# Optimization experiments

Hardware: AMD Instinct MI355X
Metric: run time of the kernel (lower is better)

The kernel has to match this reference:

```python
import jax, jax.numpy as jnp
import numpy as np

B, HW, N, C, F, ITERS = 32, 4096, 16, 128, 512, 3
EPS_LN = 1e-5
EPS_ATTN = 1e-5


def _ln(x, g, b):
    m = x.mean(-1, keepdims=True)
    v = ((x - m) ** 2).mean(-1, keepdims=True)
    return (x - m) / jnp.sqrt(v + EPS_LN) * g + b


def _gru(x, h, wih, whh, bih, bhh):
    # torch.nn.GRUCell math
    gi = x @ wih.T + bih
    gh = h @ whh.T + bhh
    i_r, i_z, i_n = jnp.split(gi, 3, axis=-1)
    h_r, h_z, h_n = jnp.split(gh, 3, axis=-1)
    r = jax.nn.sigmoid(i_r + h_r)
    z = jax.nn.sigmoid(i_z + h_z)
    n = jnp.tanh(i_n + r * h_n)
    return (1.0 - z) * n + z * h


def setup_inputs() -> dict:
    key = jax.random.key(0)
    ks = jax.random.split(key, 16)
    s = 0.02
    d = {
        'inp': jax.random.normal(ks[0], (B, HW, C), jnp.float32),
        'query': jax.random.normal(ks[1], (B, N, C), jnp.float32),
        'ln_kv_g': jnp.ones((C,), jnp.float32),
        'ln_kv_b': jnp.zeros((C,), jnp.float32),
        'Wk': jax.random.normal(ks[2], (C, C), jnp.float32) * s,
        'Wv': jax.random.normal(ks[3], (C, C), jnp.float32) * s,
        'ln_q_g': jnp.ones((C,), jnp.float32),
        'ln_q_b': jnp.zeros((C,), jnp.float32),
        'Wq': jax.random.normal(ks[4], (C, C), jnp.float32) * s,
        'gru_wih': jax.random.normal(ks[5], (3 * C, C), jnp.float32) * s,
        'gru_whh': jax.random.normal(ks[6], (3 * C, C), jnp.float32) * s,
        'gru_bih': jnp.zeros((3 * C,), jnp.float32),
        'gru_bhh': jnp.zeros((3 * C,), jnp.float32),
        'ln2_g': jnp.ones((C,), jnp.float32),
        'ln2_b': jnp.zeros((C,), jnp.float32),
        'ffn_w1': jax.random.normal(ks[7], (F, C), jnp.float32) * s,
        'ffn_b1': jnp.zeros((F,), jnp.float32),
        'ffn_w2': jax.random.normal(ks[8], (C, F), jnp.float32) * s,
        'ffn_b2': jnp.zeros((C,), jnp.float32),
    }
    return d


def reference(inp, query, ln_kv_g, ln_kv_b, Wk, Wv, ln_q_g, ln_q_b, Wq,
              gru_wih, gru_whh, gru_bih, gru_bhh, ln2_g, ln2_b,
              ffn_w1, ffn_b1, ffn_w2, ffn_b2):
    b, n, c = query.shape
    kv = _ln(inp, ln_kv_g, ln_kv_b)
    k = kv @ Wk.T  # (b, hw, c)
    v = kv @ Wv.T  # (b, hw, c)
    scale = c ** -0.5
    q = query
    a0 = None
    for _ in range(ITERS):
        x = q
        qn = _ln(q, ln_q_g, ln_q_b) @ Wq.T
        logit = jnp.einsum('bqc,bkc->bqk', qn * scale, k)  # (b, n, hw)
        a0 = jax.nn.softmax(logit, axis=1)  # inverted: softmax over slots
        a = a0 / (a0.sum(2, keepdims=True) + EPS_ATTN)  # renorm over keys
        u = jnp.einsum('bqk,bkc->bqc', a, v)
        y = _gru(u.reshape(b * n, c), x.reshape(b * n, c),
                 gru_wih, gru_whh, gru_bih, gru_bhh).reshape(b, n, c)
        z = _ln(y, ln2_g, ln2_b)
        ffn = jax.nn.relu(z @ ffn_w1.T + ffn_b1) @ ffn_w2.T + ffn_b2
        q = y + ffn
    return (q, a0)
```

## Files before the change

### kernel.cpp

```cpp
#include <hip/hip_runtime.h>
#include <math.h>

#define B_ 32
#define HW_ 4096
#define N_ 16
#define C_ 128
#define F_ 512
#define ITERS_ 3
#define EPS_LN 1e-5f
#define EPS_ATTN 1e-5f

typedef __attribute__((ext_vector_type(8))) short short8;
typedef __attribute__((ext_vector_type(4))) float f32x4;

static __device__ __forceinline__ unsigned short f2b(float f) {
    union { float f; unsigned u; } v; v.f = f;
    unsigned r = v.u + 0x7fffu + ((v.u >> 16) & 1u);
    return (unsigned short)(r >> 16);
}
static __device__ __forceinline__ float blo(unsigned u) {
    union { unsigned u; float f; } v; v.u = u << 16; return v.f;
}
static __device__ __forceinline__ float bhi(unsigned u) {
    union { unsigned u; float f; } v; v.u = u & 0xffff0000u; return v.f;
}

__global__ __launch_bounds__(256) void k_prep(
    const float* __restrict__ Wk, const float* __restrict__ Wv,
    const float* __restrict__ wih, const float* __restrict__ whh,
    const float* __restrict__ w1, const float* __restrict__ w2,
    unsigned short* __restrict__ Wk_bf, unsigned short* __restrict__ Wv_bf,
    unsigned short* __restrict__ wihT, unsigned short* __restrict__ whhT,
    unsigned short* __restrict__ w1T, unsigned short* __restrict__ w2T,
    const float* __restrict__ query, const float* __restrict__ lnqg,
    const float* __restrict__ lnqb, const float* __restrict__ Wq,
    float* __restrict__ wqTf, unsigned short* __restrict__ qn_g)
{
    __shared__ __align__(16) float xq[16 * 128];
    int tid = threadIdx.x;
    int blk = blockIdx.x;
    if (blk < 32) {
        int t = blk * 256 + tid;
        const float* src; unsigned short* dst; int off;
        if (t < 4096) { src = Wk; dst = Wk_bf; off = t; }
        else          { src = Wv; dst = Wv_bf; off = t - 4096; }
        float4 a = ((const float4*)src)[off];
        uint2 p;
        p.x = (unsigned)f2b(a.x) | ((unsigned)f2b(a.y) << 16);
        p.y = (unsigned)f2b(a.z) | ((unsigned)f2b(a.w) << 16);
        *(uint2*)(dst + off * 4) = p;
        return;
    }
    if (blk < 256) {
        const float* src; unsigned short* dst; int o, g, id, Cin;
        if (blk < 80) {
            id = (blk - 32) * 256 + tid;
            g = id / 384; o = id - g * 384;
            src = wih; dst = wihT; Cin = 128;
        } else if (blk < 128) {
            id = (blk - 80) * 256 + tid;
            g = id / 384; o = id - g * 384;
            src = whh; dst = whhT; Cin = 128;
        } else if (blk < 192) {
            id = (blk - 128) * 256 + tid;
            g = id >> 9; o = id & 511;
            src = w1; dst = w1T; Cin = 128;
        } else {
            id = (blk - 192) * 256 + tid;
            g = id >> 7; o = id & 127;
            src = w2; dst = w2T; Cin = 512;
        }
        float4 a = *(const float4*)(src + o * Cin + g * 4);
        uint2 p;
        p.x = (unsigned)f2b(a.x) | ((unsigned)f2b(a.y) << 16);
        p.y = (unsigned)f2b(a.z) | ((unsigned)f2b(a.w) << 16);
        *(uint2*)(dst + id * 4) = p;
        return;
    }
    if (blk >= 288) {
        int t = (blk - 288) * 256 + tid;
        int c = t & 127, g = t >> 7;
        float4 a = *(const float4*)(Wq + c * 128 + g * 4);
        ((float4*)wqTf)[g * 128 + c] = a;
        return;
    }
    int b = blk - 256;
    int n = tid >> 4, part = tid & 15;
    int row = b * 16 + n;
    const float4* x4 = (const float4*)(query + row * 128 + part * 8);
    float4 x0 = x4[0], x1 = x4[1];
    float s = x0.x + x0.y + x0.z + x0.w + x1.x + x1.y + x1.z + x1.w;
    float ss = x0.x * x0.x + x0.y * x0.y + x0.z * x0.z + x0.w * x0.w +
               x1.x * x1.x + x1.y * x1.y + x1.z * x1.z + x1.w * x1.w;
    s += __shfl_xor(s, 1); s += __shfl_xor(s, 2); s += __shfl_xor(s, 4); s += __shfl_xor(s, 8);
    ss += __shfl_xor(ss, 1); ss += __shfl_xor(ss, 2); ss += __shfl_xor(ss, 4); ss += __shfl_xor(ss, 8);
    float mean = s * (1.f / 128.f);
    float var = ss * (1.f / 128.f) - mean * mean;
    float rstd = rsqrtf(var + EPS_LN);
    const float4* g4 = (const float4*)(lnqg + part * 8);
    const float4* b4 = (const float4*)(lnqb + part * 8);
    float4 g0 = g4[0], g1 = g4[1], bb0 = b4[0], bb1 = b4[1];
    float4 o0, o1;
    o0.x = (x0.x - mean) * rstd * g0.x + bb0.x;
    o0.y = (x0.y - mean) * rstd * g0.y + bb0.y;
    o0.z = (x0.z - mean) * rstd * g0.z + bb0.z;
    o0.w = (x0.w - mean) * rstd * g0.w + bb0.w;
    o1.x = (x1.x - mean) * rstd * g1.x + bb1.x;
    o1.y = (x1.y - mean) * rstd * g1.y + bb1.y;
    o1.z = (x1.z - mean) * rstd * g1.z + bb1.z;
    o1.w = (x1.w - mean) * rstd * g1.w + bb1.w;
    float4* xrow = (float4*)&xq[n * 128];
    xrow[part * 2] = o0;
    xrow[part * 2 + 1] = o1;
    __syncthreads();
    float o[8] = {0.f, 0.f, 0.f, 0.f, 0.f, 0.f, 0.f, 0.f};
    const float4* xv4 = (const float4*)&xq[n * 128];
#pragma unroll 4
    for (int j = 0; j < 32; j++) {
        float4 xv = xv4[j];
#pragma unroll
        for (int i = 0; i < 8; i++) {
            float4 w = ((const float4*)(Wq + (part * 8 + i) * 128))[j];
            o[i] += w.x * xv.x + w.y * xv.y + w.z * xv.z + w.w * xv.w;
        }
    }
    const float scale = 0.08838834764831845f;
#pragma unroll
    for (int i = 0; i < 8; i++)
        qn_g[row * 128 + part * 8 + i] = f2b(o[i] * scale);
}

__global__ __launch_bounds__(256) void k_kvproj(
    const float* __restrict__ inp, const float* __restrict__ lng,
    const float* __restrict__ lnb, const unsigned short* __restrict__ Wk_bf,
    const unsigned short* __restrict__ Wv_bf, unsigned short* __restrict__ Kbf,
    unsigned short* __restrict__ Vt)
{
    __shared__ __align__(16) unsigned short W_lds[128 * 128];
    __shared__ __align__(16) unsigned short T_lds[8960];
    const int tid = threadIdx.x;
    const int wave = tid >> 6, lane = tid & 63;
    const int l15 = lane & 15, q4 = lane >> 4;
    const int kof = q4 * 8;
    const int tile0 = blockIdx.x * 64;
    const int b = tile0 >> 12;
    const int hwbase = tile0 & (HW_ - 1);

    const int srow = tid >> 1, shalf = tid & 1;
    const int sswz = srow & 7;

    float x[4][8];
    {
        const float* rowp = inp + (tile0 + (wave << 4) + l15) * C_;
        float s = 0.f, ss = 0.f;
#pragma unroll
        for (int ks = 0; ks < 4; ks++) {
#pragma unroll
            for (int h = 0; h < 2; h++) {
                float4 v = *(const float4*)(rowp + ks * 32 + kof + h * 4);
                x[ks][h * 4 + 0] = v.x; x[ks][h * 4 + 1] = v.y;
                x[ks][h * 4 + 2] = v.z; x[ks][h * 4 + 3] = v.w;
                s += v.x + v.y + v.z + v.w;
                ss += v.x * v.x + v.y * v.y + v.z * v.z + v.w * v.w;
            }
        }
        s += __shfl_xor(s, 16);  s += __shfl_xor(s, 32);
        ss += __shfl_xor(ss, 16); ss += __shfl_xor(ss, 32);
        float mean = s * (1.f / 128.f);
        float var = ss * (1.f / 128.f) - mean * mean;
        float rstd = rsqrtf(var + EPS_LN);
#pragma unroll
        for (int ks = 0; ks < 4; ks++) {
#pragma unroll
            for (int h = 0; h < 2; h++) {
                float4 g = *(const float4*)(lng + ks * 32 + kof + h * 4);
                float4 bb = *(const float4*)(lnb + ks * 32 + kof + h * 4);
                x[ks][h * 4 + 0] = (x[ks][h * 4 + 0] - mean) * rstd * g.x + bb.x;
                x[ks][h * 4 + 1] = (x[ks][h * 4 + 1] - mean) * rstd * g.y + bb.y;
                x[ks][h * 4 + 2] = (x[ks][h * 4 + 2] - mean) * rstd * g.z + bb.z;
                x[ks][h * 4 + 3] = (x[ks][h * 4 + 3] - mean) * rstd * g.w + bb.w;
            }
        }
    }
    short8 af[4];
#pragma unroll
    for (int ks = 0; ks < 4; ks++) {
        union { short8 s8; unsigned u[4]; } p;
#pragma unroll
        for (int j = 0; j < 4; j++)
            p.u[j] = (unsigned)f2b(x[ks][2 * j]) | ((unsigned)f2b(x[ks][2 * j + 1]) << 16);
        af[ks] = p.s8;
    }

    {
        const uint4* gW = (const uint4*)Wk_bf;
#pragma unroll
        for (int j = 0; j < 8; j++) {
            int c = shalf * 8 + j;
            uint4 w = gW[srow * 16 + c];
            *(uint4*)&W_lds[srow * 128 + (c ^ sswz) * 8] = w;
        }
    }
    __syncthreads();

    f32x4 acc[8];
#pragma unroll
    for (int nt = 0; nt < 8; nt++) {
        acc[nt] = (f32x4){0.f, 0.f, 0.f, 0.f};
#pragma unroll
        for (int ks = 0; ks < 4; ks++) {
            short8 bf = *(const short8*)&W_lds[(nt * 16 + l15) * 128 + ((ks * 4 + q4) ^ (l15 & 7)) * 8];
            acc[nt] = __builtin_amdgcn_mfma_f32_16x16x32_bf16(af[ks], bf, acc[nt], 0, 0, 0);
        }
    }
#pragma unroll
    for (int nt = 0; nt < 8; nt++) {
        int c = nt * 16 + l15;
#pragma unroll
        for (int i = 0; i < 4; i++)
            T_lds[((wave << 4) + (q4 << 2) + i) * 132 + c] = f2b(acc[nt][i]);
    }
    __syncthreads();
    {
        int row = tid >> 2, part = tid & 3;
        uint4* dst = (uint4*)&Kbf[(b * HW_ + hwbase + row) * C_ + part * 32];
#pragma unroll
        for (int j = 0; j < 4; j++)
            dst[j] = *(const uint4*)&T_lds[row * 132 + part * 32 + j * 8];
    }
    {
        const uint4* gW = (const uint4*)Wv_bf;
#pragma unroll
        for (int j = 0; j < 8; j++) {
            int c = shalf * 8 + j;
            uint4 w = gW[srow * 16 + c];
            *(uint4*)&W_lds[srow * 128 + (c ^ sswz) * 8] = w;
        }
    }
    __syncthreads();
#pragma unroll
    for (int nt = 0; nt < 8; nt++) {
        acc[nt] = (f32x4){0.f, 0.f, 0.f, 0.f};
#pragma unroll
        for (int ks = 0; ks < 4; ks++) {
            short8 bf = *(const short8*)&W_lds[(nt * 16 + l15) * 128 + ((ks * 4 + q4) ^ (l15 & 7)) * 8];
            acc[nt] = __builtin_amdgcn_mfma_f32_16x16x32_bf16(af[ks], bf, acc[nt], 0, 0, 0);
        }
    }
    __syncthreads();
#pragma unroll
    for (int nt = 0; nt < 8; nt++) {
        int c = nt * 16 + l15;
#pragma unroll
        for (int i = 0; i < 4; i++)
            T_lds[c * 70 + (wave << 4) + (q4 << 2) + i] = f2b(acc[nt][i]);
    }
    __syncthreads();
    {
        int c = tid >> 1, half = tid & 1;
        uint4* dst = (uint4*)&Vt[(b * C_ + c) * HW_ + hwbase + half * 32];
#pragma unroll
        for (int j = 0; j < 4; j++)
            dst[j] = *(const uint4*)&T_lds[c * 70 + half * 32 + j * 8];
    }
}

__global__ __launch_bounds__(256) void k_attn(
    const unsigned short* __restrict__ qn_g, const unsigned short* __restrict__ Kbf,
    const unsigned short* __restrict__ Vt, float* __restrict__ Upart,
    float* __restrict__ rspart, float* __restrict__ a0_out, int last)
{
    __shared__ __align__(16) float Ul[4][16 * 132];
    __shared__ __align__(16) unsigned short Pb[4][16 * 40];
    __shared__ float rsw[4][16];
    const int b = blockIdx.y, chunk = blockIdx.x;
    const int tid = threadIdx.x;
    const int wave = tid >> 6, lane = tid & 63;
    const int l15 = lane & 15, q4 = lane >> 4;
    const int kof = q4 * 8;
    const int hwb = chunk * 128 + wave * 32;

    short8 aq[4];
#pragma unroll
    for (int ks = 0; ks < 4; ks++)
        aq[ks] = *(const short8*)&qn_g[(b * 16 + l15) * 128 + ks * 32 + kof];
    short8 av[8];
#pragma unroll
    for (int ct = 0; ct < 8; ct++)
        av[ct] = *(const short8*)&Vt[(b * C_ + ct * 16 + l15) * HW_ + hwb + kof];

    unsigned short* Pw = &Pb[wave][0];
    float rs[4] = {0.f, 0.f, 0.f, 0.f};
#pragma unroll
    for (int s = 0; s < 2; s++) {
        int hwt = hwb + s * 16;
        f32x4 sa = {0.f, 0.f, 0.f, 0.f};
#pragma unroll
        for (int ks = 0; ks < 4; ks++) {
            short8 bk = *(const short8*)&Kbf[(b * HW_ + hwt + l15) * C_ + ks * 32 + kof];
            sa = __builtin_amdgcn_mfma_f32_16x16x32_bf16(aq[ks], bk, sa, 0, 0, 0);
        }
        float mx = fmaxf(fmaxf(sa[0], sa[1]), fmaxf(sa[2], sa[3]));
        mx = fmaxf(mx, __shfl_xor(mx, 16));
        mx = fmaxf(mx, __shfl_xor(mx, 32));
        float e[4]; float ssum = 0.f;
#pragma unroll
        for (int i = 0; i < 4; i++) { e[i] = __expf(sa[i] - mx); ssum += e[i]; }
        ssum += __shfl_xor(ssum, 16);
        ssum += __shfl_xor(ssum, 32);
        float inv = 1.f / ssum;
#pragma unroll
        for (int i = 0; i < 4; i++) {
            float a0v = e[i] * inv;
            rs[i] += a0v;
            if (last) a0_out[(b * 16 + q4 * 4 + i) * HW_ + hwt + l15] = a0v;
            Pw[(q4 * 4 + i) * 40 + s * 16 + l15] = f2b(a0v);
        }
    }
#pragma unroll
    for (int i = 0; i < 4; i++) {
        rs[i] += __shfl_xor(rs[i], 1);
        rs[i] += __shfl_xor(rs[i], 2);
        rs[i] += __shfl_xor(rs[i], 4);
        rs[i] += __shfl_xor(rs[i], 8);
    }
    if (l15 == 0) {
#pragma unroll
        for (int i = 0; i < 4; i++) rsw[wave][q4 * 4 + i] = rs[i];
    }
    short8 bp = *(const short8*)&Pw[l15 * 40 + kof];
#pragma unroll
    for (int ct = 0; ct < 8; ct++) {
        f32x4 ua = __builtin_amdgcn_mfma_f32_16x16x32_bf16(av[ct], bp, (f32x4){0.f, 0.f, 0.f, 0.f}, 0, 0, 0);
        *(f32x4*)&Ul[wave][l15 * 132 + ct * 16 + (q4 << 2)] = ua;
    }
    __syncthreads();
    {
        float* up = Upart + (b * 32 + chunk) * 2048;
#pragma unroll
        for (int k = 0; k < 8; k++) {
            int idx = tid + k * 256;
            int q = idx >> 7, c = idx & 127;
            up[idx] = Ul[0][q * 132 + c] + Ul[1][q * 132 + c] +
                      Ul[2][q * 132 + c] + Ul[3][q * 132 + c];
        }
        if (tid < 16)
            rspart[(b * 32 + chunk) * 16 + tid] =
                rsw[0][tid] + rsw[1][tid] + rsw[2][tid] + rsw[3][tid];
    }
}

__global__ __launch_bounds__(1024, 4) void k_tail(
    const float* __restrict__ Upart, const float* __restrict__ rspart,
    const float* __restrict__ hsrc, float* __restrict__ q_buf,
    const unsigned short* __restrict__ wihT, const unsigned short* __restrict__ whhT,
    const float* __restrict__ bih, const float* __restrict__ bhh,
    const float* __restrict__ ln2g, const float* __restrict__ ln2b,
    const unsigned short* __restrict__ w1T, const float* __restrict__ b1,
    const unsigned short* __restrict__ w2T, const float* __restrict__ b2,
    const float* __restrict__ lnqg, const float* __restrict__ lnqb,
    const float* __restrict__ wqTf, unsigned short* __restrict__ qn_g,
    float* __restrict__ out_q, int last)
{
    __shared__ __align__(16) float red[1024];
    __shared__ __align__(16) float u_l[128];
    __shared__ __align__(16) float h_l[128];
    __shared__ __align__(16) float y_l[128];
    __shared__ __align__(16) float z_l[128];
    __shared__ __align__(16) float g_l[768];
    __shared__ __align__(16) float h1_l[512];
    __shared__ float srs;
    const int tid = threadIdx.x;
    const int row = blockIdx.x;
    const int b = row >> 4, q = row & 15;

    {
        int c = tid & 127, h = tid >> 7;
        const float* up = Upart + (b * 32 + h * 4) * 2048 + q * 128 + c;
        float part = 0.f;
#pragma unroll
        for (int ch = 0; ch < 4; ch++) part += up[ch * 2048];
        red[tid] = part;
        if (tid < 128) h_l[tid] = hsrc[row * 128 + tid];
        if (tid >= 128 && tid < 160) {
            int t = tid - 128;
            float v = rspart[(b * 32 + t) * 16 + q];
            v += __shfl_xor(v, 1); v += __shfl_xor(v, 2); v += __shfl_xor(v, 4);
            v += __shfl_xor(v, 8); v += __shfl_xor(v, 16);
            if (t == 0) srs = v;
        }
    }
    __syncthreads();
    if (tid < 128) {
        float s = 0.f;
#pragma unroll
        for (int h = 0; h < 8; h++) s += red[tid + 128 * h];
        u_l[tid] = s / (srs + EPS_ATTN);
    }
    __syncthreads();
    if (tid < 768) {
        int o = tid;
        const uint2* wp;
        const float* src;
        float bias;
        if (o < 384) { wp = (const uint2*)wihT + o; src = u_l; bias = bih[o]; }
        else         { wp = (const uint2*)whhT + (o - 384); src = h_l; bias = bhh[o - 384]; }
        float acc = 0.f;
#pragma unroll 4
        for (int g = 0; g < 32; g++) {
            uint2 w = wp[g * 384];
            float4 sv = *(const float4*)&src[g * 4];
            acc += blo(w.x) * sv.x + bhi(w.x) * sv.y
                 + blo(w.y) * sv.z + bhi(w.y) * sv.w;
        }
        g_l[o] = acc + bias;
    }
    __syncthreads();
    if (tid < 128) {
        int c = tid;
        float ir = g_l[c], iz = g_l[128 + c], in_ = g_l[256 + c];
        float hr = g_l[384 + c], hz = g_l[512 + c], hn = g_l[640 + c];
        float rr = 1.f / (1.f + expf(-(ir + hr)));
        float zz = 1.f / (1.f + expf(-(iz + hz)));
        float nn = tanhf(in_ + rr * hn);
        y_l[c] = (1.f - zz) * nn + zz * h_l[c];
    }
    __syncthreads();
    {
        int l = tid & 63;
        float v0 = y_l[l], v1 = y_l[l + 64];
        float s = v0 + v1, ss = v0 * v0 + v1 * v1;
#pragma unroll
        for (int off = 1; off < 64; off <<= 1) {
            s += __shfl_xor(s, off);
            ss += __shfl_xor(ss, off);
        }
        float mean = s * (1.f / 128.f);
        float var = ss * (1.f / 128.f) - mean * mean;
        float rstd = rsqrtf(var + EPS_LN);
        if (tid < 128)
            z_l[tid] = (y_l[tid] - mean) * rstd * ln2g[tid] + ln2b[tid];
    }
    __syncthreads();
    {
        int f = tid & 511, hh = tid >> 9;
        const uint2* wp = (const uint2*)w1T + f;
        float acc = 0.f;
#pragma unroll 4
        for (int j = 0; j < 16; j++) {
            int g = hh * 16 + j;
            uint2 w = wp[g * 512];
            float4 zv = *(const float4*)&z_l[g * 4];
            acc += blo(w.x) * zv.x + bhi(w.x) * zv.y
                 + blo(w.y) * zv.z + bhi(w.y) * zv.w;
        }
        red[tid] = acc;
    }
    __syncthreads();
    if (tid < 512)
        h1_l[tid] = fmaxf(red[tid] + red[tid + 512] + b1[tid], 0.f);
    __syncthreads();
    {
        int c = tid & 127, h8 = tid >> 7;
        const uint2* wp = (const uint2*)w2T + c;
        float acc = 0.f;
#pragma unroll 4
        for (int j = 0; j < 16; j++) {
            int g = h8 * 16 + j;
            uint2 w = wp[g * 128];
            float4 hv = *(const float4*)&h1_l[g * 4];
            acc += blo(w.x) * hv.x + bhi(w.x) * hv.y
                 + blo(w.y) * hv.z + bhi(w.y) * hv.w;
        }
        red[tid] = acc;
    }
    __syncthreads();
    if (tid < 128) {
        float f2 = 0.f;
#pragma unroll
        for (int k = 0; k < 8; k++) f2 += red[tid + 128 * k];
        float qn = y_l[tid] + f2 + b2[tid];
        u_l[tid] = qn;
        q_buf[row * 128 + tid] = qn;
        if (last) out_q[row * 128 + tid] = qn;
    }
    if (last) return;
    __syncthreads();
    {
        int l = tid & 63;
        float v0 = u_l[l], v1 = u_l[l + 64];
        float s = v0 + v1, ss = v0 * v0 + v1 * v1;
#pragma unroll
        for (int off = 1; off < 64; off <<= 1) {
            s += __shfl_xor(s, off);
            ss += __shfl_xor(ss, off);
        }
        float mean = s * (1.f / 128.f);
        float var = ss * (1.f / 128.f) - mean * mean;
        float rstd = rsqrtf(var + EPS_LN);
        if (tid < 128)
            z_l[tid] = (u_l[tid] - mean) * rstd * lnqg[tid] + lnqb[tid];
    }
    __syncthreads();
    {
        int c = tid & 127, h8 = tid >> 7;
        const float4* wp = (const float4*)wqTf + c;
        float acc = 0.f;
#pragma unroll
        for (int j = 0; j < 4; j++) {
            int g = h8 * 4 + j;
            float4 w = wp[g * 128];
            float4 zv = *(const float4*)&z_l[g * 4];
            acc += w.x * zv.x + w.y * zv.y + w.z * zv.z + w.w * zv.w;
        }
        red[tid] = acc;
    }
    __syncthreads();
    if (tid < 128) {
        float qa = 0.f;
#pragma unroll
        for (int k = 0; k < 8; k++) qa += red[tid + 128 * k];
        qn_g[row * 128 + tid] = f2b(qa * 0.08838834764831845f);
    }
}

extern "C" void kernel_launch(void* const* d_in, const int* in_sizes, int n_in,
                              void* d_out, int out_size, void* d_ws, size_t ws_size,
                              hipStream_t stream) {
    const float* inp     = (const float*)d_in[0];
    const float* query   = (const float*)d_in[1];
    const float* ln_kv_g = (const float*)d_in[2];
    const float* ln_kv_b = (const float*)d_in[3];
    const float* Wk      = (const float*)d_in[4];
    const float* Wv      = (const float*)d_in[5];
    const float* ln_q_g  = (const float*)d_in[6];
    const float* ln_q_b  = (const float*)d_in[7];
    const float* Wq      = (const float*)d_in[8];
    const float* gru_wih = (const float*)d_in[9];
    const float* gru_whh = (const float*)d_in[10];
    const float* gru_bih = (const float*)d_in[11];
    const float* gru_bhh = (const float*)d_in[12];
    const float* ln2_g   = (const float*)d_in[13];
    const float* ln2_b   = (const float*)d_in[14];
    const float* ffn_w1  = (const float*)d_in[15];
    const float* ffn_b1  = (const float*)d_in[16];
    const float* ffn_w2  = (const float*)d_in[17];
    const float* ffn_b2  = (const float*)d_in[18];

    char* ws = (char*)d_ws;
    unsigned short* Kbf    = (unsigned short*)ws;
    unsigned short* Vt     = (unsigned short*)(ws + 33554432);
    float* q_buf           = (float*)(ws + 67108864);
    float* Upart           = (float*)(ws + 67371008);
    float* rspart          = (float*)(ws + 75759616);
    unsigned short* qn_g   = (unsigned short*)(ws + 75825152);
    unsigned short* Wk_bf  = (unsigned short*)(ws + 75956224);
    unsigned short* Wv_bf  = (unsigned short*)(ws + 75988992);
    unsigned short* wihT   = (unsigned short*)(ws + 76021760);
    unsigned short* whhT   = (unsigned short*)(ws + 76120064);
    unsigned short* w1T    = (unsigned short*)(ws + 76218368);
    unsigned short* w2T    = (unsigned short*)(ws + 76349440);
    float* wqTf            = (float*)(ws + 76480512);

    float* out_q  = (float*)d_out;
    float* out_a0 = out_q + B_ * N_ * C_;

    k_prep<<<dim3(304), dim3(256), 0, stream>>>(
        Wk, Wv, gru_wih, gru_whh, ffn_w1, ffn_w2,
        Wk_bf, Wv_bf, wihT, whhT, w1T, w2T,
        query, ln_q_g, ln_q_b, Wq, wqTf, qn_g);
    k_kvproj<<<dim3((B_ * HW_) / 64), dim3(256), 0, stream>>>(
        inp, ln_kv_g, ln_kv_b, Wk_bf, Wv_bf, Kbf, Vt);

    for (int it = 0; it < ITERS_; it++) {
        int last = (it == ITERS_ - 1) ? 1 : 0;
        const float* hsrc = (it == 0) ? query : q_buf;
        k_attn<<<dim3(32, B_), dim3(256), 0, stream>>>(
            qn_g, Kbf, Vt, Upart, rspart, out_a0, last);
        k_tail<<<dim3(B_ * N_), dim3(1024), 0, stream>>>(
            Upart, rspart, hsrc, q_buf, wihT, whhT, gru_bih, gru_bhh,
            ln2_g, ln2_b, w1T, ffn_b1, w2T, ffn_b2,
            ln_q_g, ln_q_b, wqTf, qn_g, out_q, last);
    }
}
```

Baseline: 296.6 us.

## Pre-swizzle K/V weights and load them into LDS with global_load_lds in 512-thread tiles

k_prep now writes Wk/Wv in bf16 already in the XOR-swizzled LDS layout, so k_kvproj can copy them straight from global memory into LDS with global_load_lds, without a pass through registers. The projection block doubles to 512 threads and 128 rows per tile, which halves how often each block reloads the weights. The V transpose buffer is widened and one barrier is removed. The main risks are higher LDS use per block, which may lower occupancy, and correct ordering of the asynchronous LDS writes relative to the existing barriers.

Result: faster. 287.1 us (-3.2%).

```diff
diff --git a/kernel.cpp b/kernel.cpp
--- a/kernel.cpp
+++ b/kernel.cpp
@@ -24,12 +24,17 @@
 static __device__ __forceinline__ float bhi(unsigned u) {
     union { unsigned u; float f; } v; v.u = u & 0xffff0000u; return v.f;
 }
+static __device__ __forceinline__ void gload_lds16(const void* g, void* l) {
+    __builtin_amdgcn_global_load_lds(
+        (const __attribute__((address_space(1))) unsigned int*)g,
+        (__attribute__((address_space(3))) unsigned int*)l, 16, 0, 0);
+}
 
 __global__ __launch_bounds__(256) void k_prep(
     const float* __restrict__ Wk, const float* __restrict__ Wv,
     const float* __restrict__ wih, const float* __restrict__ whh,
     const float* __restrict__ w1, const float* __restrict__ w2,
-    unsigned short* __restrict__ Wk_bf, unsigned short* __restrict__ Wv_bf,
+    unsigned short* __restrict__ Wk_sw, unsigned short* __restrict__ Wv_sw,
     unsigned short* __restrict__ wihT, unsigned short* __restrict__ whhT,
     unsigned short* __restrict__ w1T, unsigned short* __restrict__ w2T,
     const float* __restrict__ query, const float* __restrict__ lnqg,
@@ -42,13 +47,17 @@
     if (blk < 32) {
         int t = blk * 256 + tid;
         const float* src; unsigned short* dst; int off;
-        if (t < 4096) { src = Wk; dst = Wk_bf; off = t; }
-        else          { src = Wv; dst = Wv_bf; off = t - 4096; }
+        if (t < 4096) { src = Wk; dst = Wk_sw; off = t; }
+        else          { src = Wv; dst = Wv_sw; off = t - 4096; }
         float4 a = ((const float4*)src)[off];
         uint2 p;
         p.x = (unsigned)f2b(a.x) | ((unsigned)f2b(a.y) << 16);
         p.y = (unsigned)f2b(a.z) | ((unsigned)f2b(a.w) << 16);
-        *(uint2*)(dst + off * 4) = p;
+        int r = off >> 5;
+        int j = off & 31;
+        int cg = j >> 1, half = j & 1;
+        int dsw = r * 128 + (((cg ^ (r & 7)) << 3)) + (half << 2);
+        *(uint2*)(dst + dsw) = p;
         return;
     }
     if (blk < 256) {
@@ -130,24 +139,29 @@
         qn_g[row * 128 + part * 8 + i] = f2b(o[i] * scale);
 }
 
-__global__ __launch_bounds__(256) void k_kvproj(
+__global__ __launch_bounds__(512, 4) void k_kvproj(
     const float* __restrict__ inp, const float* __restrict__ lng,
-    const float* __restrict__ lnb, const unsigned short* __restrict__ Wk_bf,
-    const unsigned short* __restrict__ Wv_bf, unsigned short* __restrict__ Kbf,
+    const float* __restrict__ lnb, const unsigned short* __restrict__ Wk_sw,
+    const unsigned short* __restrict__ Wv_sw, unsigned short* __restrict__ Kbf,
     unsigned short* __restrict__ Vt)
 {
     __shared__ __align__(16) unsigned short W_lds[128 * 128];
-    __shared__ __align__(16) unsigned short T_lds[8960];
+    __shared__ __align__(16) unsigned short T_lds[128 * 132];
     const int tid = threadIdx.x;
     const int wave = tid >> 6, lane = tid & 63;
     const int l15 = lane & 15, q4 = lane >> 4;
     const int kof = q4 * 8;
-    const int tile0 = blockIdx.x * 64;
+    const int tile0 = blockIdx.x * 128;
     const int b = tile0 >> 12;
     const int hwbase = tile0 & (HW_ - 1);
 
-    const int srow = tid >> 1, shalf = tid & 1;
-    const int sswz = srow & 7;
+    {
+        const char* gw = (const char*)Wk_sw + wave * 4096 + lane * 16;
+        char* lw = (char*)W_lds + wave * 4096;
+#pragma unroll
+        for (int j = 0; j < 4; j++)
+            gload_lds16(gw + j * 1024, lw + j * 1024);
+    }
 
     float x[4][8];
     {
@@ -192,15 +206,6 @@
         af[ks] = p.s8;
     }
 
-    {
-        const uint4* gW = (const uint4*)Wk_bf;
-#pragma unroll
-        for (int j = 0; j < 8; j++) {
-            int c = shalf * 8 + j;
-            uint4 w = gW[srow * 16 + c];
-            *(uint4*)&W_lds[srow * 128 + (c ^ sswz) * 8] = w;
-        }
-    }
     __syncthreads();
 
     f32x4 acc[8];
@@ -221,6 +226,7 @@
             T_lds[((wave << 4) + (q4 << 2) + i) * 132 + c] = f2b(acc[nt][i]);
     }
     __syncthreads();
+
     {
         int row = tid >> 2, part = tid & 3;
         uint4* dst = (uint4*)&Kbf[(b * HW_ + hwbase + row) * C_ + part * 32];
@@ -229,15 +235,14 @@
             dst[j] = *(const uint4*)&T_lds[row * 132 + part * 32 + j * 8];
     }
     {
-        const uint4* gW = (const uint4*)Wv_bf;
-#pragma unroll
-        for (int j = 0; j < 8; j++) {
-            int c = shalf * 8 + j;
-            uint4 w = gW[srow * 16 + c];
-            *(uint4*)&W_lds[srow * 128 + (c ^ sswz) * 8] = w;
-        }
-    }
-    __syncthreads();
+        const char* gw = (const char*)Wv_sw + wave * 4096 + lane * 16;
+        char* lw = (char*)W_lds + wave * 4096;
+#pragma unroll
+        for (int j = 0; j < 4; j++)
+            gload_lds16(gw + j * 1024, lw + j * 1024);
+    }
+    __syncthreads();
+
 #pragma unroll
     for (int nt = 0; nt < 8; nt++) {
         acc[nt] = (f32x4){0.f, 0.f, 0.f, 0.f};
@@ -247,21 +252,21 @@
             acc[nt] = __builtin_amdgcn_mfma_f32_16x16x32_bf16(af[ks], bf, acc[nt], 0, 0, 0);
         }
     }
-    __syncthreads();
 #pragma unroll
     for (int nt = 0; nt < 8; nt++) {
         int c = nt * 16 + l15;
 #pragma unroll
         for (int i = 0; i < 4; i++)
-            T_lds[c * 70 + (wave << 4) + (q4 << 2) + i] = f2b(acc[nt][i]);
-    }
-    __syncthreads();
-    {
-        int c = tid >> 1, half = tid & 1;
-        uint4* dst = (uint4*)&Vt[(b * C_ + c) * HW_ + hwbase + half * 32];
+            T_lds[c * 132 + (wave << 4) + (q4 << 2) + i] = f2b(acc[nt][i]);
+    }
+    __syncthreads();
+
+    {
+        int c = tid >> 2, part = tid & 3;
+        uint4* dst = (uint4*)&Vt[(b * C_ + c) * HW_ + hwbase + part * 32];
 #pragma unroll
         for (int j = 0; j < 4; j++)
-            dst[j] = *(const uint4*)&T_lds[c * 70 + half * 32 + j * 8];
+            dst[j] = *(const uint4*)&T_lds[c * 132 + part * 32 + j * 8];
     }
 }
 
@@ -554,8 +559,8 @@
     float* Upart           = (float*)(ws + 67371008);
     float* rspart          = (float*)(ws + 75759616);
     unsigned short* qn_g   = (unsigned short*)(ws + 75825152);
-    unsigned short* Wk_bf  = (unsigned short*)(ws + 75956224);
-    unsigned short* Wv_bf  = (unsigned short*)(ws + 75988992);
+    unsigned short* Wk_sw  = (unsigned short*)(ws + 75956224);
+    unsigned short* Wv_sw  = (unsigned short*)(ws + 75988992);
     unsigned short* wihT   = (unsigned short*)(ws + 76021760);
     unsigned short* whhT   = (unsigned short*)(ws + 76120064);
     unsigned short* w1T    = (unsigned short*)(ws + 76218368);
@@ -567,10 +572,10 @@
 
     k_prep<<<dim3(304), dim3(256), 0, stream>>>(
         Wk, Wv, gru_wih, gru_whh, ffn_w1, ffn_w2,
-        Wk_bf, Wv_bf, wihT, whhT, w1T, w2T,
+        Wk_sw, Wv_sw, wihT, whhT, w1T, w2T,
         query, ln_q_g, ln_q_b, Wq, wqTf, qn_g);
-    k_kvproj<<<dim3((B_ * HW_) / 64), dim3(256), 0, stream>>>(
-        inp, ln_kv_g, ln_kv_b, Wk_bf, Wv_bf, Kbf, Vt);
+    k_kvproj<<<dim3((B_ * HW_) / 128), dim3(512), 0, stream>>>(
+        inp, ln_kv_g, ln_kv_b, Wk_sw, Wv_sw, Kbf, Vt);
 
     for (int it = 0; it < ITERS_; it++) {
         int last = (it == ITERS_ - 1) ? 1 : 0;
```
